# Kernel optimization log

Measured on AMD Instinct MI355X. Metric: run time of the kernel, lower is better.

## Reference

```python
import jax, jax.numpy as jnp
import numpy as np

EMBED = 1024
HEADS = 16
HEAD_DIM = EMBED // HEADS


def setup_inputs() -> dict:
    key = jax.random.key(0)
    ks = jax.random.split(key, 9)
    s = 0.02
    return {
        "hidden_states": jax.random.normal(ks[0], (1, 4, 1500, EMBED), dtype=jnp.float32),
        "q_w": jax.random.normal(ks[1], (EMBED, EMBED), dtype=jnp.float32) * s,
        "q_b": jax.random.normal(ks[2], (EMBED,), dtype=jnp.float32) * s,
        "k_w": jax.random.normal(ks[3], (EMBED, EMBED), dtype=jnp.float32) * s,
        "v_w": jax.random.normal(ks[4], (EMBED, EMBED), dtype=jnp.float32) * s,
        "v_b": jax.random.normal(ks[5], (EMBED,), dtype=jnp.float32) * s,
        "out_w": jax.random.normal(ks[6], (EMBED, EMBED), dtype=jnp.float32) * s,
        "out_b": jax.random.normal(ks[7], (EMBED,), dtype=jnp.float32) * s,
    }


def reference(hidden_states, q_w, q_b, k_w, v_w, v_b, out_w, out_b):
    # hidden_states: [1, B, S, E]
    _, bsz, tgt_len, _ = hidden_states.shape
    x = hidden_states[0]  # [B, S, E]
    scaling = HEAD_DIM ** -0.5

    def split_heads(t):  # [B, S, E] -> [B, H, S, Dh]
        return t.reshape(bsz, tgt_len, HEADS, HEAD_DIM).transpose(0, 2, 1, 3)

    # Linear layers use torch convention: y = x @ W.T + b  (k_proj has no bias)
    q = split_heads((x @ q_w.T + q_b) * scaling)
    k = split_heads(x @ k_w.T)
    v = split_heads(x @ v_w.T + v_b)

    # attention scores [B, H, S, S]
    attn_weights = jnp.einsum("bhqd,bhkd->bhqk", q, k)
    attn_probs = jax.nn.softmax(attn_weights, axis=-1)
    attn_out = jnp.einsum("bhqk,bhkd->bhqd", attn_probs, v)  # [B, H, S, Dh]

    attn_out = attn_out.transpose(0, 2, 1, 3).reshape(1, bsz, tgt_len, EMBED)
    return attn_out @ out_w.T + out_b
```

## Files before the change

kernel.cpp:

```cpp
#include <hip/hip_runtime.h>
#include <cstddef>
#include <cstdint>

#define EMB 1024
#define SEQ 1500
#define NB 4
#define NH 16
#define DH 64
#define MTOT (NB*SEQ)
#define VTS 1536

typedef __bf16 bf16;
typedef __bf16 bf16x4 __attribute__((ext_vector_type(4)));
typedef __bf16 bf16x8 __attribute__((ext_vector_type(8)));
typedef short  s16x4  __attribute__((ext_vector_type(4)));
typedef float  f32x4  __attribute__((ext_vector_type(4)));

#define LOG2E 1.44269504088896340736f

__device__ __forceinline__ void async16(const void* g, const void* l) {
    __builtin_amdgcn_global_load_lds(
        (const __attribute__((address_space(1))) uint32_t*)g,
        (__attribute__((address_space(3))) uint32_t*)l, 16, 0, 0);
}

struct CvtArgs {
    const float* xs; bf16* xd;
    const float* w[4]; bf16* wd[4];
};

__global__ __launch_bounds__(256) void cvt_kernel(CvtArgs a) {
    const size_t NX = (size_t)MTOT * EMB;
    const size_t NW = (size_t)EMB * EMB;
    const size_t tot = NX + 4 * NW;
    for (size_t i = ((size_t)blockIdx.x * 256 + threadIdx.x) * 4; i < tot;
         i += (size_t)gridDim.x * 1024) {
        const float* s; bf16* d; size_t off;
        if (i < NX) { s = a.xs; d = a.xd; off = i; }
        else {
            size_t j = i - NX;
            int wi = (int)(j >> 20);
            off = j & (NW - 1);
            s = a.w[wi]; d = a.wd[wi];
        }
        float4 v = *(const float4*)(s + off);
        bf16x4 o = { (bf16)v.x, (bf16)v.y, (bf16)v.z, (bf16)v.w };
        *(bf16x4*)(d + off) = o;
    }
}

__global__ __launch_bounds__(256) void gemm_fused(
    const bf16* __restrict__ X,
    const bf16* __restrict__ W0, const bf16* __restrict__ W1, const bf16* __restrict__ W2,
    const float* __restrict__ b_q, const float* __restrict__ b_v, const float* __restrict__ b_o,
    bf16* __restrict__ Oq, bf16* __restrict__ Ok, bf16* __restrict__ Ovt,
    float* __restrict__ Of, int M, int qkv)
{
    __shared__ bf16 As[2][128 * 32];
    __shared__ bf16 Bs[2][128 * 32];
    const int tid = threadIdx.x;
    const int lane = tid & 63, w = tid >> 6;
    const int q = lane >> 4, lr = lane & 15;
    const int wr = w >> 1, wc = w & 1;

    const int id = blockIdx.x;
    const int t_ = id >> 3;
    const int mtile = (id & 7) + (t_ % 6) * 8;
    const int y = t_ / 6;
    const int m0 = mtile * 128;

    int proj, n0;
    if (qkv) { proj = y >> 3; n0 = (y & 7) * 128; }
    else     { proj = 3;      n0 = y * 128; }

    const bf16 *PA, *PB;
    int baseA, baseB, limA, limB;
    if (proj == 2) {
        PA = X;  baseA = m0; limA = M;
        PB = W2; baseB = n0; limB = EMB;
    } else {
        PA = (proj == 0) ? W0 : (proj == 1 ? W1 : W0);
        baseA = n0; limA = EMB;
        PB = X; baseB = m0; limB = M;
    }

    f32x4 acc[4][4] = {};

    const int srow = w * 32 + (lane >> 2);
    const int swz_ch = (((lane & 3) ^ ((lane >> 3) & 3))) * 8;
    const bf16* pA[2]; const bf16* pB[2];
#pragma unroll
    for (int i = 0; i < 2; i++) {
        int ra = baseA + srow + i * 16; ra = ra < limA ? ra : limA - 1;
        int rb = baseB + srow + i * 16; rb = rb < limB ? rb : limB - 1;
        pA[i] = PA + (size_t)ra * EMB + swz_ch;
        pB[i] = PB + (size_t)rb * EMB + swz_ch;
    }

#pragma unroll
    for (int i = 0; i < 2; i++) {
        async16(pA[i], As[0] + (w * 2 + i) * 512);
        async16(pB[i], Bs[0] + (w * 2 + i) * 512);
    }

    const int qsw = (q ^ ((lr >> 1) & 3)) * 8;
    const int arow = (wr * 64 + lr) * 32;
    const int brow = (wc * 64 + lr) * 32;

    for (int k0 = 0; k0 < EMB; k0 += 32) {
        const int cur = (k0 >> 5) & 1;
        __syncthreads();
        const int nxt = k0 + 32;
        if (nxt < EMB) {
#pragma unroll
            for (int i = 0; i < 2; i++) {
                async16(pA[i] + nxt, As[cur ^ 1] + (w * 2 + i) * 512);
                async16(pB[i] + nxt, Bs[cur ^ 1] + (w * 2 + i) * 512);
            }
        }
        const bf16* Ab = As[cur];
        const bf16* Bb = Bs[cur];
        bf16x8 af[4], bfr[4];
#pragma unroll
        for (int t = 0; t < 4; t++) {
            af[t]  = *(const bf16x8*)(Ab + arow + t * 512 + qsw);
            bfr[t] = *(const bf16x8*)(Bb + brow + t * 512 + qsw);
        }
#pragma unroll
        for (int ti = 0; ti < 4; ti++)
#pragma unroll
            for (int tj = 0; tj < 4; tj++)
                acc[ti][tj] = __builtin_amdgcn_mfma_f32_16x16x32_bf16(
                    af[ti], bfr[tj], acc[ti][tj], 0, 0, 0);
    }

    if (proj <= 1) {
        const float scale = (proj == 0) ? 0.125f * LOG2E : 1.0f;
        const float* bias = (proj == 0) ? b_q : nullptr;
        bf16* O = (proj == 0) ? Oq : Ok;
#pragma unroll
        for (int tj = 0; tj < 4; tj++) {
            const int m = m0 + wc * 64 + tj * 16 + lr;
            if (m >= M) continue;
            const int b_ = m / SEQ, s_ = m % SEQ;
#pragma unroll
            for (int ti = 0; ti < 4; ti++) {
                const int nb = n0 + wr * 64 + ti * 16 + q * 4;
                const int h = nb >> 6, d = nb & 63;
                float4 b4 = bias ? *(const float4*)(bias + nb)
                                 : make_float4(0.f, 0.f, 0.f, 0.f);
                bf16x4 o;
                o[0] = (bf16)((acc[ti][tj][0] + b4.x) * scale);
                o[1] = (bf16)((acc[ti][tj][1] + b4.y) * scale);
                o[2] = (bf16)((acc[ti][tj][2] + b4.z) * scale);
                o[3] = (bf16)((acc[ti][tj][3] + b4.w) * scale);
                *(bf16x4*)(O + (((size_t)b_ * NH + h) * SEQ + s_) * DH + d) = o;
            }
        }
    } else if (proj == 2) {
#pragma unroll
        for (int ti = 0; ti < 4; ti++) {
            const int mb = m0 + wr * 64 + ti * 16 + q * 4;
            if (mb >= M) continue;
            const int b_ = mb / SEQ, s_ = mb % SEQ;
#pragma unroll
            for (int tj = 0; tj < 4; tj++) {
                const int nb = n0 + wc * 64 + tj * 16 + lr;
                const int h = nb >> 6, d = nb & 63;
                const float bv = b_v[nb];
                bf16x4 o;
                o[0] = (bf16)(acc[ti][tj][0] + bv);
                o[1] = (bf16)(acc[ti][tj][1] + bv);
                o[2] = (bf16)(acc[ti][tj][2] + bv);
                o[3] = (bf16)(acc[ti][tj][3] + bv);
                *(bf16x4*)(Ovt + ((size_t)(b_ * NH + h) * DH + d) * VTS + s_) = o;
            }
        }
    } else {
#pragma unroll
        for (int tj = 0; tj < 4; tj++) {
            const int m = m0 + wc * 64 + tj * 16 + lr;
            if (m >= M) continue;
#pragma unroll
            for (int ti = 0; ti < 4; ti++) {
                const int nb = n0 + wr * 64 + ti * 16 + q * 4;
                const float4 b4 = *(const float4*)(b_o + nb);
                float4 o;
                o.x = acc[ti][tj][0] + b4.x;
                o.y = acc[ti][tj][1] + b4.y;
                o.z = acc[ti][tj][2] + b4.z;
                o.w = acc[ti][tj][3] + b4.w;
                *(float4*)(Of + (size_t)m * EMB + nb) = o;
            }
        }
    }
}

__global__ __launch_bounds__(256) void attn_mfma(
    const bf16* __restrict__ Qb, const bf16* __restrict__ Kb,
    const bf16* __restrict__ Vt, bf16* __restrict__ ctx)
{
    __shared__ bf16 Ks[64][72];
    __shared__ bf16 Vs[64][72];
    const int tid = threadIdx.x;
    const int lane = tid & 63, w = tid >> 6;
    const int q = lane >> 4, lr = lane & 15;
    const int bh = blockIdx.x, b_ = bh >> 4, h_ = bh & 15;
    const int q0 = blockIdx.y * 128;
    const size_t base = (size_t)bh * SEQ * DH;
    const size_t vbase = (size_t)bh * DH * VTS;

    int qrow[2];
    bf16x8 qf[2][2];
#pragma unroll
    for (int g = 0; g < 2; g++) {
        qrow[g] = q0 + g * 64 + w * 16 + lr;
        const int qrc = qrow[g] < SEQ ? qrow[g] : (SEQ - 1);
        qf[g][0] = *(const bf16x8*)(Qb + base + (size_t)qrc * DH + q * 8);
        qf[g][1] = *(const bf16x8*)(Qb + base + (size_t)qrc * DH + 32 + q * 8);
    }

    f32x4 oacc[2][4] = {};
    float lsum[2] = {0.f, 0.f};

    const int srow = tid >> 3;
    const int sch  = (tid & 7) * 8;

    const int NT = (SEQ + 63) / 64;

    uint4 ka, kb, va, vb;
    {
        int g0 = srow;
        int g1 = 32 + srow;
        ka = *(const uint4*)(Kb + base + (size_t)g0 * DH + sch);
        kb = *(const uint4*)(Kb + base + (size_t)g1 * DH + sch);
        va = *(const uint4*)(Vt + vbase + (size_t)srow * VTS + sch);
        vb = *(const uint4*)(Vt + vbase + (size_t)(srow + 32) * VTS + sch);
    }

    for (int kt = 0; kt < NT; kt++) {
        const int k0 = kt * 64;
        __syncthreads();
        *(uint4*)&Ks[srow][sch]      = ka;
        *(uint4*)&Ks[srow + 32][sch] = kb;
        *(uint4*)&Vs[srow][sch]      = va;
        *(uint4*)&Vs[srow + 32][sch] = vb;
        __syncthreads();

        if (kt + 1 < NT) {
            const int n0_ = k0 + 64;
            int g0 = n0_ + srow;      g0 = g0 < SEQ ? g0 : (SEQ - 1);
            int g1 = n0_ + 32 + srow; g1 = g1 < SEQ ? g1 : (SEQ - 1);
            ka = *(const uint4*)(Kb + base + (size_t)g0 * DH + sch);
            kb = *(const uint4*)(Kb + base + (size_t)g1 * DH + sch);
            va = *(const uint4*)(Vt + vbase + (size_t)srow * VTS + n0_ + sch);
            vb = *(const uint4*)(Vt + vbase + (size_t)(srow + 32) * VTS + n0_ + sch);
        }

        bf16x8 kf[2][4];
#pragma unroll
        for (int s = 0; s < 2; s++)
#pragma unroll
            for (int mt = 0; mt < 4; mt++)
                kf[s][mt] = *(const bf16x8*)(&Ks[mt * 16 + lr][s * 32 + q * 8]);

        s16x4 pf[2][4];
#pragma unroll
        for (int g = 0; g < 2; g++) {
            f32x4 st[4] = {};
#pragma unroll
            for (int s = 0; s < 2; s++)
#pragma unroll
                for (int mt = 0; mt < 4; mt++)
                    st[mt] = __builtin_amdgcn_mfma_f32_16x16x32_bf16(
                        kf[s][mt], qf[g][s], st[mt], 0, 0, 0);

            if (k0 + 64 > SEQ) {
#pragma unroll
                for (int mt = 0; mt < 4; mt++)
#pragma unroll
                    for (int r = 0; r < 4; r++)
                        if (k0 + mt * 16 + q * 4 + r >= SEQ) st[mt][r] = -1e30f;
            }

            float ps = lsum[g];
#pragma unroll
            for (int mt = 0; mt < 4; mt++) {
                bf16x4 pb;
#pragma unroll
                for (int r = 0; r < 4; r++) {
                    const float p = exp2f(st[mt][r]);
                    ps += p;
                    pb[r] = (bf16)p;
                }
                pf[g][mt] = __builtin_bit_cast(s16x4, pb);
            }
            lsum[g] = ps;
        }

#pragma unroll
        for (int c = 0; c < 4; c++) {
#pragma unroll
            for (int dt = 0; dt < 4; dt++) {
                const s16x4 vf = __builtin_bit_cast(s16x4,
                    *(const bf16x4*)(&Vs[dt * 16 + lr][c * 16 + q * 4]));
                oacc[0][dt] = __builtin_amdgcn_mfma_f32_16x16x16bf16_1k(
                    vf, pf[0][c], oacc[0][dt], 0, 0, 0);
                oacc[1][dt] = __builtin_amdgcn_mfma_f32_16x16x16bf16_1k(
                    vf, pf[1][c], oacc[1][dt], 0, 0, 0);
            }
        }
    }

#pragma unroll
    for (int g = 0; g < 2; g++) {
        float l = lsum[g];
        l += __shfl_xor(l, 16, 64);
        l += __shfl_xor(l, 32, 64);
        const float inv = 1.0f / l;
        if (qrow[g] < SEQ) {
            const size_t rowoff = ((size_t)b_ * SEQ + qrow[g]) * EMB + h_ * DH;
#pragma unroll
            for (int dt = 0; dt < 4; dt++) {
                bf16x4 o;
#pragma unroll
                for (int r = 0; r < 4; r++) o[r] = (bf16)(oacc[g][dt][r] * inv);
                *(bf16x4*)(ctx + rowoff + dt * 16 + q * 4) = o;
            }
        }
    }
}

extern "C" void kernel_launch(void* const* d_in, const int* in_sizes, int n_in,
                              void* d_out, int out_size, void* d_ws, size_t ws_size,
                              hipStream_t stream) {
    const float* x     = (const float*)d_in[0];
    const float* q_w   = (const float*)d_in[1];
    const float* q_b   = (const float*)d_in[2];
    const float* k_w   = (const float*)d_in[3];
    const float* v_w   = (const float*)d_in[4];
    const float* v_b   = (const float*)d_in[5];
    const float* out_w = (const float*)d_in[6];
    const float* out_b = (const float*)d_in[7];
    float* out = (float*)d_out;

    const size_t nbuf = (size_t)MTOT * EMB;
    const size_t nvt  = (size_t)NB * NH * DH * VTS;
    const size_t nw   = (size_t)EMB * EMB;
    bf16* xb  = (bf16*)d_ws;
    bf16* qws = xb  + nbuf;
    bf16* kws = qws + nbuf;
    bf16* vtw = kws + nbuf;
    bf16* wqb = vtw + nvt;
    bf16* wkb = wqb + nw;
    bf16* wvb = wkb + nw;
    bf16* wob = wvb + nw;
    bf16* ctx = xb;

    CvtArgs ca;
    ca.xs = x;      ca.xd = xb;
    ca.w[0] = q_w;  ca.wd[0] = wqb;
    ca.w[1] = k_w;  ca.wd[1] = wkb;
    ca.w[2] = v_w;  ca.wd[2] = wvb;
    ca.w[3] = out_w; ca.wd[3] = wob;
    cvt_kernel<<<dim3(2560), 256, 0, stream>>>(ca);

    gemm_fused<<<dim3(48 * 24), 256, 0, stream>>>(
        xb, wqb, wkb, wvb, q_b, v_b, nullptr, qws, kws, vtw, nullptr, MTOT, 1);

    attn_mfma<<<dim3(NB * NH, (SEQ + 127) / 128), 256, 0, stream>>>(qws, kws, vtw, ctx);

    gemm_fused<<<dim3(48 * 8), 256, 0, stream>>>(
        ctx, wob, nullptr, nullptr, nullptr, nullptr, out_b,
        nullptr, nullptr, nullptr, out, MTOT, 0);
}
```

Measured before the change: 260.9 us.

## Add 64-row out-proj GEMM, async double-buffered attention loads, MFMA row sums

The output projection moves from the shared 128x128 GEMM into a dedicated 64x128-tile kernel. This roughly doubles the block count for better CU occupancy, and the kernel uses async global-to-LDS loads with double buffering. The attention kernel replaces register-staged K/V loads with double-buffered global_load_lds into XOR-swizzled LDS, removing one barrier per tile. It also computes softmax denominators with an MFMA against a ones vector and packs probabilities to bf16 by truncation using raw exp2. The trade-offs are truncated probabilities, a different masked-logit sentinel, and doubled LDS use in attention.

```diff
diff --git a/kernel.cpp b/kernel.cpp
--- a/kernel.cpp
+++ b/kernel.cpp
@@ -22,6 +22,11 @@
     __builtin_amdgcn_global_load_lds(
         (const __attribute__((address_space(1))) uint32_t*)g,
         (__attribute__((address_space(3))) uint32_t*)l, 16, 0, 0);
+}
+
+__device__ __forceinline__ uint32_t pack_bf16_trunc(float e0, float e1) {
+    return __builtin_amdgcn_perm(__builtin_bit_cast(uint32_t, e1),
+                                 __builtin_bit_cast(uint32_t, e0), 0x07060302u);
 }
 
 struct CvtArgs {
@@ -52,9 +57,9 @@
 __global__ __launch_bounds__(256) void gemm_fused(
     const bf16* __restrict__ X,
     const bf16* __restrict__ W0, const bf16* __restrict__ W1, const bf16* __restrict__ W2,
-    const float* __restrict__ b_q, const float* __restrict__ b_v, const float* __restrict__ b_o,
+    const float* __restrict__ b_q, const float* __restrict__ b_v,
     bf16* __restrict__ Oq, bf16* __restrict__ Ok, bf16* __restrict__ Ovt,
-    float* __restrict__ Of, int M, int qkv)
+    int M)
 {
     __shared__ bf16 As[2][128 * 32];
     __shared__ bf16 Bs[2][128 * 32];
@@ -68,10 +73,8 @@
     const int mtile = (id & 7) + (t_ % 6) * 8;
     const int y = t_ / 6;
     const int m0 = mtile * 128;
-
-    int proj, n0;
-    if (qkv) { proj = y >> 3; n0 = (y & 7) * 128; }
-    else     { proj = 3;      n0 = y * 128; }
+    const int proj = y >> 3;
+    const int n0 = (y & 7) * 128;
 
     const bf16 *PA, *PB;
     int baseA, baseB, limA, limB;
@@ -79,7 +82,7 @@
         PA = X;  baseA = m0; limA = M;
         PB = W2; baseB = n0; limB = EMB;
     } else {
-        PA = (proj == 0) ? W0 : (proj == 1 ? W1 : W0);
+        PA = (proj == 0) ? W0 : W1;
         baseA = n0; limA = EMB;
         PB = X; baseB = m0; limB = M;
     }
@@ -157,7 +160,7 @@
                 *(bf16x4*)(O + (((size_t)b_ * NH + h) * SEQ + s_) * DH + d) = o;
             }
         }
-    } else if (proj == 2) {
+    } else {
 #pragma unroll
         for (int ti = 0; ti < 4; ti++) {
             const int mb = m0 + wr * 64 + ti * 16 + q * 4;
@@ -176,22 +179,72 @@
                 *(bf16x4*)(Ovt + ((size_t)(b_ * NH + h) * DH + d) * VTS + s_) = o;
             }
         }
-    } else {
-#pragma unroll
-        for (int tj = 0; tj < 4; tj++) {
-            const int m = m0 + wc * 64 + tj * 16 + lr;
-            if (m >= M) continue;
-#pragma unroll
-            for (int ti = 0; ti < 4; ti++) {
-                const int nb = n0 + wr * 64 + ti * 16 + q * 4;
-                const float4 b4 = *(const float4*)(b_o + nb);
-                float4 o;
-                o.x = acc[ti][tj][0] + b4.x;
-                o.y = acc[ti][tj][1] + b4.y;
-                o.z = acc[ti][tj][2] + b4.z;
-                o.w = acc[ti][tj][3] + b4.w;
-                *(float4*)(Of + (size_t)m * EMB + nb) = o;
-            }
+    }
+}
+
+__global__ __launch_bounds__(256) void gemm_out64(
+    const bf16* __restrict__ X, const bf16* __restrict__ Wo,
+    const float* __restrict__ b_o, float* __restrict__ Of, int M)
+{
+    __shared__ bf16 Ws[2][128 * 32];
+    __shared__ bf16 Xs[2][64 * 32];
+    const int tid = threadIdx.x;
+    const int lane = tid & 63, w = tid >> 6;
+    const int q = lane >> 4, lr = lane & 15;
+    const int wm = w & 1, wn = w >> 1;
+    const int m0 = blockIdx.x * 64, n0 = blockIdx.y * 128;
+
+    const int srow = tid >> 2;
+    const int sch8 = ((tid & 3) ^ ((tid >> 3) & 3)) * 8;
+    int xr = m0 + srow; if (xr >= M) xr = M - 1;
+    const bf16* pX  = X  + (size_t)xr * EMB + sch8;
+    const bf16* pW0 = Wo + (size_t)(n0 + srow) * EMB + sch8;
+    const bf16* pW1 = Wo + (size_t)(n0 + 64 + srow) * EMB + sch8;
+
+    async16(pW0, Ws[0] + tid * 8);
+    async16(pW1, Ws[0] + tid * 8 + 2048);
+    async16(pX,  Xs[0] + tid * 8);
+
+    f32x4 acc[4][2] = {};
+    const int fsw = (q ^ ((lr >> 1) & 3)) * 8;
+
+    for (int k0 = 0; k0 < EMB; k0 += 32) {
+        const int cur = (k0 >> 5) & 1;
+        __syncthreads();
+        if (k0 + 32 < EMB) {
+            async16(pW0 + k0 + 32, Ws[cur ^ 1] + tid * 8);
+            async16(pW1 + k0 + 32, Ws[cur ^ 1] + tid * 8 + 2048);
+            async16(pX  + k0 + 32, Xs[cur ^ 1] + tid * 8);
+        }
+        bf16x8 wf[4], xf[2];
+#pragma unroll
+        for (int t = 0; t < 4; t++)
+            wf[t] = *(const bf16x8*)(Ws[cur] + (wn * 64 + t * 16 + lr) * 32 + fsw);
+#pragma unroll
+        for (int t = 0; t < 2; t++)
+            xf[t] = *(const bf16x8*)(Xs[cur] + (wm * 32 + t * 16 + lr) * 32 + fsw);
+#pragma unroll
+        for (int ti = 0; ti < 4; ti++)
+#pragma unroll
+            for (int tj = 0; tj < 2; tj++)
+                acc[ti][tj] = __builtin_amdgcn_mfma_f32_16x16x32_bf16(
+                    wf[ti], xf[tj], acc[ti][tj], 0, 0, 0);
+    }
+
+#pragma unroll
+    for (int tj = 0; tj < 2; tj++) {
+        const int m = m0 + wm * 32 + tj * 16 + lr;
+        if (m >= M) continue;
+#pragma unroll
+        for (int ti = 0; ti < 4; ti++) {
+            const int nb = n0 + wn * 64 + ti * 16 + q * 4;
+            const float4 b4 = *(const float4*)(b_o + nb);
+            float4 o;
+            o.x = acc[ti][tj][0] + b4.x;
+            o.y = acc[ti][tj][1] + b4.y;
+            o.z = acc[ti][tj][2] + b4.z;
+            o.w = acc[ti][tj][3] + b4.w;
+            *(float4*)(Of + (size_t)m * EMB + nb) = o;
         }
     }
 }
@@ -200,8 +253,8 @@
     const bf16* __restrict__ Qb, const bf16* __restrict__ Kb,
     const bf16* __restrict__ Vt, bf16* __restrict__ ctx)
 {
-    __shared__ bf16 Ks[64][72];
-    __shared__ bf16 Vs[64][72];
+    __shared__ bf16 Ks[2][64 * 64];
+    __shared__ bf16 Vs[2][64 * 64];
     const int tid = threadIdx.x;
     const int lane = tid & 63, w = tid >> 6;
     const int q = lane >> 4, lr = lane & 15;
@@ -221,48 +274,50 @@
     }
 
     f32x4 oacc[2][4] = {};
-    float lsum[2] = {0.f, 0.f};
+    f32x4 lacc[2] = {};
+    const s16x4 ones = { (short)0x3F80, (short)0x3F80, (short)0x3F80, (short)0x3F80 };
 
     const int srow = tid >> 3;
-    const int sch  = (tid & 7) * 8;
+    const int sch8 = ((tid & 7) ^ (srow & 7)) * 8;
+    const int kswz = lr & 7;
 
     const int NT = (SEQ + 63) / 64;
 
-    uint4 ka, kb, va, vb;
     {
-        int g0 = srow;
-        int g1 = 32 + srow;
-        ka = *(const uint4*)(Kb + base + (size_t)g0 * DH + sch);
-        kb = *(const uint4*)(Kb + base + (size_t)g1 * DH + sch);
-        va = *(const uint4*)(Vt + vbase + (size_t)srow * VTS + sch);
-        vb = *(const uint4*)(Vt + vbase + (size_t)(srow + 32) * VTS + sch);
+        int r0 = srow, r1 = srow + 32;
+        async16(Kb + base + (size_t)r0 * DH + sch8, Ks[0] + tid * 8);
+        async16(Kb + base + (size_t)r1 * DH + sch8, Ks[0] + tid * 8 + 2048);
+        async16(Vt + vbase + (size_t)srow * VTS + sch8,        Vs[0] + tid * 8);
+        async16(Vt + vbase + (size_t)(srow + 32) * VTS + sch8, Vs[0] + tid * 8 + 2048);
     }
 
     for (int kt = 0; kt < NT; kt++) {
         const int k0 = kt * 64;
+        const int cur = kt & 1;
         __syncthreads();
-        *(uint4*)&Ks[srow][sch]      = ka;
-        *(uint4*)&Ks[srow + 32][sch] = kb;
-        *(uint4*)&Vs[srow][sch]      = va;
-        *(uint4*)&Vs[srow + 32][sch] = vb;
-        __syncthreads();
 
         if (kt + 1 < NT) {
-            const int n0_ = k0 + 64;
-            int g0 = n0_ + srow;      g0 = g0 < SEQ ? g0 : (SEQ - 1);
-            int g1 = n0_ + 32 + srow; g1 = g1 < SEQ ? g1 : (SEQ - 1);
-            ka = *(const uint4*)(Kb + base + (size_t)g0 * DH + sch);
-            kb = *(const uint4*)(Kb + base + (size_t)g1 * DH + sch);
-            va = *(const uint4*)(Vt + vbase + (size_t)srow * VTS + n0_ + sch);
-            vb = *(const uint4*)(Vt + vbase + (size_t)(srow + 32) * VTS + n0_ + sch);
-        }
+            const int kn = k0 + 64;
+            int r0 = kn + srow;      if (r0 >= SEQ) r0 = SEQ - 1;
+            int r1 = kn + srow + 32; if (r1 >= SEQ) r1 = SEQ - 1;
+            async16(Kb + base + (size_t)r0 * DH + sch8, Ks[cur ^ 1] + tid * 8);
+            async16(Kb + base + (size_t)r1 * DH + sch8, Ks[cur ^ 1] + tid * 8 + 2048);
+            async16(Vt + vbase + (size_t)srow * VTS + kn + sch8,
+                    Vs[cur ^ 1] + tid * 8);
+            async16(Vt + vbase + (size_t)(srow + 32) * VTS + kn + sch8,
+                    Vs[cur ^ 1] + tid * 8 + 2048);
+        }
+
+        const bf16* Kc = Ks[cur];
+        const bf16* Vc = Vs[cur];
 
         bf16x8 kf[2][4];
 #pragma unroll
         for (int s = 0; s < 2; s++)
 #pragma unroll
             for (int mt = 0; mt < 4; mt++)
-                kf[s][mt] = *(const bf16x8*)(&Ks[mt * 16 + lr][s * 32 + q * 8]);
+                kf[s][mt] = *(const bf16x8*)(Kc + (mt * 16 + lr) * 64 +
+                                             ((4 * s + q) ^ kswz) * 8);
 
         s16x4 pf[2][4];
 #pragma unroll
@@ -280,22 +335,24 @@
                 for (int mt = 0; mt < 4; mt++)
 #pragma unroll
                     for (int r = 0; r < 4; r++)
-                        if (k0 + mt * 16 + q * 4 + r >= SEQ) st[mt][r] = -1e30f;
-            }
-
-            float ps = lsum[g];
+                        if (k0 + mt * 16 + q * 4 + r >= SEQ) st[mt][r] = -16384.0f;
+            }
+
 #pragma unroll
             for (int mt = 0; mt < 4; mt++) {
-                bf16x4 pb;
-#pragma unroll
-                for (int r = 0; r < 4; r++) {
-                    const float p = exp2f(st[mt][r]);
-                    ps += p;
-                    pb[r] = (bf16)p;
-                }
-                pf[g][mt] = __builtin_bit_cast(s16x4, pb);
-            }
-            lsum[g] = ps;
+                float e0 = __builtin_amdgcn_exp2f(st[mt][0]);
+                float e1 = __builtin_amdgcn_exp2f(st[mt][1]);
+                float e2 = __builtin_amdgcn_exp2f(st[mt][2]);
+                float e3 = __builtin_amdgcn_exp2f(st[mt][3]);
+                uint32_t lo = pack_bf16_trunc(e0, e1);
+                uint32_t hi = pack_bf16_trunc(e2, e3);
+                uint2 pk = { lo, hi };
+                pf[g][mt] = __builtin_bit_cast(s16x4, pk);
+            }
+#pragma unroll
+            for (int c = 0; c < 4; c++)
+                lacc[g] = __builtin_amdgcn_mfma_f32_16x16x16bf16_1k(
+                    ones, pf[g][c], lacc[g], 0, 0, 0);
         }
 
 #pragma unroll
@@ -303,7 +360,8 @@
 #pragma unroll
             for (int dt = 0; dt < 4; dt++) {
                 const s16x4 vf = __builtin_bit_cast(s16x4,
-                    *(const bf16x4*)(&Vs[dt * 16 + lr][c * 16 + q * 4]));
+                    *(const bf16x4*)(Vc + (dt * 16 + lr) * 64 +
+                                     ((2 * c + (q >> 1)) ^ kswz) * 8 + (q & 1) * 4));
                 oacc[0][dt] = __builtin_amdgcn_mfma_f32_16x16x16bf16_1k(
                     vf, pf[0][c], oacc[0][dt], 0, 0, 0);
                 oacc[1][dt] = __builtin_amdgcn_mfma_f32_16x16x16bf16_1k(
@@ -314,10 +372,7 @@
 
 #pragma unroll
     for (int g = 0; g < 2; g++) {
-        float l = lsum[g];
-        l += __shfl_xor(l, 16, 64);
-        l += __shfl_xor(l, 32, 64);
-        const float inv = 1.0f / l;
+        const float inv = 1.0f / lacc[g][0];
         if (qrow[g] < SEQ) {
             const size_t rowoff = ((size_t)b_ * SEQ + qrow[g]) * EMB + h_ * DH;
 #pragma unroll
@@ -366,11 +421,9 @@
     cvt_kernel<<<dim3(2560), 256, 0, stream>>>(ca);
 
     gemm_fused<<<dim3(48 * 24), 256, 0, stream>>>(
-        xb, wqb, wkb, wvb, q_b, v_b, nullptr, qws, kws, vtw, nullptr, MTOT, 1);
+        xb, wqb, wkb, wvb, q_b, v_b, qws, kws, vtw, MTOT);
 
     attn_mfma<<<dim3(NB * NH, (SEQ + 127) / 128), 256, 0, stream>>>(qws, kws, vtw, ctx);
 
-    gemm_fused<<<dim3(48 * 8), 256, 0, stream>>>(
-        ctx, wob, nullptr, nullptr, nullptr, nullptr, out_b,
-        nullptr, nullptr, nullptr, out, MTOT, 0);
-}
+    gemm_out64<<<dim3((MTOT + 63) / 64, 8), 256, 0, stream>>>(ctx, wob, out_b, out, MTOT);
+}
```

Result: faster. 240.6 us (-7.8%).
